# Performance work log

Measured on AMD Instinct MI355X. Metric: run time of the kernel, lower is better.

The kernel has to match this reference:

```python
import jax, jax.numpy as jnp
import numpy as np

HEADS = 8
NEG_SLOPE = 0.2


def _leaky(x):
    return jnp.where(x >= 0, x, NEG_SLOPE * x)


def _layernorm(x, g, b):
    # torch nn.LayerNorm over last dim, eps=1e-5, biased variance
    m = x.mean(-1, keepdims=True)
    v = ((x - m) ** 2).mean(-1, keepdims=True)
    return (x - m) / jnp.sqrt(v + 1e-5) * g + b


def _batchnorm(x, g, b):
    # training-mode BatchNorm2d, eps=1e-4, biased variance over (N,H,W)
    m = x.mean((0, 2, 3), keepdims=True)
    v = ((x - m) ** 2).mean((0, 2, 3), keepdims=True)
    return (x - m) / jnp.sqrt(v + 1e-4) * g[None, :, None, None] + b[None, :, None, None]


def _depthwise3x3(x, k):
    # x: (B,C,H,W), k: (C,1,3,3) depthwise kernel
    C = x.shape[1]
    return jax.lax.conv_general_dilated(
        x, k, (1, 1), 'SAME', feature_group_count=C,
        dimension_numbers=('NCHW', 'OIHW', 'NCHW'))


def _attn_layer(x, wq, wk, wv, wproj, bproj, wpos):
    # x: (B,H,W,C) channels-last; MDTA-style transposed attention
    b, H, W, C = x.shape
    d = C // HEADS
    xf = x.reshape(b, H * W, C)
    q, k, v = xf @ wq, xf @ wk, xf @ wv  # (b, n, C)

    def split(t):
        return t.reshape(b, H * W, HEADS, d).transpose(0, 2, 3, 1)  # (b, h, d, n)

    qh, kh, vh = split(q), split(k), split(v)
    # F.normalize over token axis n (eps=1e-12)
    qn = qh / jnp.maximum(jnp.sqrt((qh * qh).sum(-1, keepdims=True)), 1e-12)
    kn = kh / jnp.maximum(jnp.sqrt((kh * kh).sum(-1, keepdims=True)), 1e-12)
    attn = jax.nn.softmax(jnp.einsum('bhdn,bhen->bhde', kn, qn), axis=-1)  # (b,h,d,d)
    o = jnp.einsum('bhde,bhen->bhdn', attn, vh)  # (b,h,d,n)
    o = o.transpose(0, 3, 1, 2).reshape(b, H * W, C)
    out_c = (o @ wproj + bproj).reshape(b, H, W, C)
    out_p = _depthwise3x3(v.reshape(b, H, W, C).transpose(0, 3, 1, 2), wpos).transpose(0, 2, 3, 1)
    return out_c * out_p


def _transformer_block(x, wq, wk, wv, wproj, bproj, wpos, ln_g, ln_b, wff):
    # x: NCHW -> BHWC, 2 (attn + prenorm-FF) residual blocks, -> NCHW
    x = x.transpose(0, 2, 3, 1)
    for i in range(wq.shape[0]):
        x = _attn_layer(x, wq[i], wk[i], wv[i], wproj[i], bproj[i], wpos[i]) + x
        x = _layernorm(x, ln_g[i], ln_b[i]) @ wff[i] + x
    return x.transpose(0, 3, 1, 2)


def _saa(x, w1, w2):
    # SAA_Block: 8x8 spatial pool, global min-max norm, bmm correlation, SE gating
    b, c, H, W = x.shape
    y = x.reshape(b, c, 8, H // 8, 8, W // 8).mean((3, 5)).reshape(b, c, 64)
    y = (y - y.min()) / (y.max() - y.min())
    y = jnp.einsum('bci,bdi->bcd', y, y).mean(2)[:, :, None, None]  # (b,c,1,1)
    g = (x * y).mean((2, 3))  # (b,c) global avg pool
    g = jax.nn.sigmoid(_leaky(g @ w1) @ w2)
    return x * g[:, :, None, None]


def setup_inputs() -> dict:
    key = jax.random.key(0)
    B, C, H, W = 16, 64, 128, 128
    L = 2  # num_blocks in Transformer_block
    ks = jax.random.split(key, 12)
    s = 0.05
    inp = {
        'x': jax.random.normal(ks[0], (B, C, H, W), jnp.float32),
        'wq': jax.random.normal(ks[1], (L, C, C), jnp.float32) * s,
        'wk': jax.random.normal(ks[2], (L, C, C), jnp.float32) * s,
        'wv': jax.random.normal(ks[3], (L, C, C), jnp.float32) * s,
        'wproj': jax.random.normal(ks[4], (L, C, C), jnp.float32) * s,
        'bproj': jnp.zeros((L, C), jnp.float32),
        'wpos': jax.random.normal(ks[5], (L, C, 1, 3, 3), jnp.float32) * s,
        'ln_g': jnp.ones((L, C), jnp.float32),
        'ln_b': jnp.zeros((L, C), jnp.float32),
        'wff': jax.random.normal(ks[6], (L, C, C), jnp.float32) * s,
        'bn1_g': jnp.ones((C,), jnp.float32),
        'bn1_b': jnp.zeros((C,), jnp.float32),
        'wd': jax.random.normal(ks[7], (C, C), jnp.float32) * s,
        'bn2_g': jnp.ones((C,), jnp.float32),
        'bn2_b': jnp.zeros((C,), jnp.float32),
        'saa_w1': jax.random.normal(ks[8], (C, C // 16), jnp.float32) * s,
        'saa_w2': jax.random.normal(ks[9], (C // 16, C), jnp.float32) * s,
    }
    return inp


def reference(x, wq, wk, wv, wproj, bproj, wpos, ln_g, ln_b, wff,
              bn1_g, bn1_b, wd, bn2_g, bn2_b, saa_w1, saa_w2):
    # res path: C (Transformer_block) -> L -> B -> D (1x1 conv) -> L -> B
    r = _transformer_block(x, wq, wk, wv, wproj, bproj, wpos, ln_g, ln_b, wff)
    r = _batchnorm(_leaky(r), bn1_g, bn1_b)
    r = jnp.einsum('bchw,co->bohw', r, wd)  # 1x1 conv, bias=False
    r = _batchnorm(_leaky(r), bn2_g, bn2_b)
    return _saa(r + x, saa_w1, saa_w2)
```

## Files before the change

kernel.cpp:

```cpp
#include <hip/hip_runtime.h>

constexpr int NB = 16, NC = 64, NH = 128, NW = 128;
constexpr int NPIX = NH * NW;
constexpr int NTOT = NB * NPIX;
constexpr size_t BUF = (size_t)NTOT * NC;

constexpr size_t OFF_A   = 0;
constexpr size_t OFF_ACT = BUF;
constexpr size_t OFF_V   = 2 * BUF;
constexpr size_t OFF_S   = 3 * BUF;
constexpr size_t OFF_QSQ = OFF_S   + 2*16*512;
constexpr size_t OFF_KSQ = OFF_QSQ + 2048;
constexpr size_t OFF_BN1 = OFF_KSQ + 2048;
constexpr size_t OFF_BN2 = OFF_BN1 + 128;
constexpr size_t ZERO_FLOATS = 16384 + 2048 + 2048 + 128 + 128;
constexpr size_t OFF_W2  = OFF_BN2 + 128;
constexpr size_t OFF_AB1 = OFF_W2  + 131072;
constexpr size_t OFF_AB2 = OFF_AB1 + 128;
constexpr size_t OFF_Y   = OFF_AB2 + 128;
constexpr size_t OFF_GATE= OFF_Y   + 65536;

__device__ __forceinline__ float leaky(float x) { return x >= 0.f ? x : 0.2f * x; }

__global__ __launch_bounds__(256) void k_transpose_in(const float* __restrict__ x,
                                                      float* __restrict__ A) {
  __shared__ float t[64][65];
  int blk = blockIdx.x;
  int b = blk >> 8;
  int p0 = (blk & 255) * 64;
  int tid = threadIdx.x;
  int cq = tid >> 6, p = tid & 63;
  for (int i = 0; i < 16; i++) {
    int c = cq * 16 + i;
    t[p][c] = x[((size_t)(b * 64 + c)) * NPIX + p0 + p];
  }
  __syncthreads();
  int pq = tid >> 6, c = tid & 63;
  for (int i = 0; i < 16; i++) {
    int p2 = pq * 16 + i;
    A[((size_t)(b * NPIX + p0 + p2)) * 64 + c] = t[p2][c];
  }
}

__global__ __launch_bounds__(256) void k_mat_v(const float* __restrict__ act,
                                               const float* __restrict__ wv,
                                               float* __restrict__ v, int l) {
  int gpix = blockIdx.x * 256 + threadIdx.x;
  const float* xr = act + (size_t)gpix * 64;
  const float* W = wv + (size_t)l * 4096;
  float* out = v + (size_t)gpix * 64;
#pragma unroll 1
  for (int jc = 0; jc < 4; jc++) {
    float acc[16];
#pragma unroll
    for (int j = 0; j < 16; j++) acc[j] = 0.f;
#pragma unroll 1
    for (int cc = 0; cc < 4; cc++) {
      const float4 x0 = *(const float4*)(xr + cc * 16);
      const float4 x1 = *(const float4*)(xr + cc * 16 + 4);
      const float4 x2 = *(const float4*)(xr + cc * 16 + 8);
      const float4 x3 = *(const float4*)(xr + cc * 16 + 12);
      const float xv[16] = {x0.x,x0.y,x0.z,x0.w, x1.x,x1.y,x1.z,x1.w,
                            x2.x,x2.y,x2.z,x2.w, x3.x,x3.y,x3.z,x3.w};
#pragma unroll
      for (int ci = 0; ci < 16; ci++) {
        const float* wrow = W + (cc * 16 + ci) * 64 + jc * 16;
#pragma unroll
        for (int j = 0; j < 16; j++) acc[j] = fmaf(xv[ci], wrow[j], acc[j]);
      }
    }
    float4 o0 = {acc[0], acc[1], acc[2], acc[3]};
    float4 o1 = {acc[4], acc[5], acc[6], acc[7]};
    float4 o2 = {acc[8], acc[9], acc[10], acc[11]};
    float4 o3 = {acc[12], acc[13], acc[14], acc[15]};
    *(float4*)(out + jc * 16)      = o0;
    *(float4*)(out + jc * 16 + 4)  = o1;
    *(float4*)(out + jc * 16 + 8)  = o2;
    *(float4*)(out + jc * 16 + 12) = o3;
  }
}

__global__ __launch_bounds__(256) void k_qk_stats(const float* __restrict__ act,
    const float* __restrict__ wq, const float* __restrict__ wk,
    float* __restrict__ S, float* __restrict__ qsq, float* __restrict__ ksq, int l) {
  int wave = (blockIdx.x * 256 + threadIdx.x) >> 6;
  int lane = threadIdx.x & 63;
  int b = wave >> 7, hh = wave & 127;
  const float* Wq = wq + (size_t)l * 4096;
  const float* Wk = wk + (size_t)l * 4096;
  float wqc[64], wkc[64];
#pragma unroll
  for (int ci = 0; ci < 64; ci++) {
    wqc[ci] = Wq[ci * 64 + lane];
    wkc[ci] = Wk[ci * 64 + lane];
  }
  float Sacc[8];
#pragma unroll
  for (int e = 0; e < 8; e++) Sacc[e] = 0.f;
  float qsa = 0.f, ksa = 0.f;
  int gbase = lane & 56;
  const float* rowp = act + ((size_t)(b * NPIX + hh * NW)) * 64;
#pragma unroll 1
  for (int w = 0; w < 128; w++) {
    const float* xp = rowp + w * 64;
    float q = 0.f, k = 0.f;
#pragma unroll
    for (int ci = 0; ci < 64; ci++) {
      float xv = xp[ci];
      q = fmaf(xv, wqc[ci], q);
      k = fmaf(xv, wkc[ci], k);
    }
    qsa = fmaf(q, q, qsa);
    ksa = fmaf(k, k, ksa);
#pragma unroll
    for (int e = 0; e < 8; e++) {
      float qe = __shfl(q, gbase + e, 64);
      Sacc[e] = fmaf(k, qe, Sacc[e]);
    }
  }
  float* Sb = S + ((size_t)l * 16 + b) * 512 + lane * 8;
#pragma unroll
  for (int e = 0; e < 8; e++) atomicAdd(Sb + e, Sacc[e]);
  atomicAdd(qsq + ((size_t)l * 16 + b) * 64 + lane, qsa);
  atomicAdd(ksq + ((size_t)l * 16 + b) * 64 + lane, ksa);
}

__global__ __launch_bounds__(64) void k_attn(const float* __restrict__ S,
    const float* __restrict__ qsq, const float* __restrict__ ksq,
    const float* __restrict__ wproj, float* __restrict__ W2, int l) {
  int b = blockIdx.x, t = threadIdx.x;
  __shared__ float A[8][8][8];
  const float* Sb = S + ((size_t)l * 16 + b) * 512;
  const float* qs = qsq + ((size_t)l * 16 + b) * 64;
  const float* ks = ksq + ((size_t)l * 16 + b) * 64;
  int h = t >> 3, d = t & 7;
  float kden = fmaxf(sqrtf(ks[h * 8 + d]), 1e-12f);
  float pre[8];
  float mx = -1e30f;
#pragma unroll
  for (int e = 0; e < 8; e++) {
    float qden = fmaxf(sqrtf(qs[h * 8 + e]), 1e-12f);
    pre[e] = Sb[(h * 8 + d) * 8 + e] / (kden * qden);
    mx = fmaxf(mx, pre[e]);
  }
  float sum = 0.f;
#pragma unroll
  for (int e = 0; e < 8; e++) { pre[e] = expf(pre[e] - mx); sum += pre[e]; }
  float inv = 1.f / sum;
#pragma unroll
  for (int e = 0; e < 8; e++) A[h][d][e] = pre[e] * inv;
  __syncthreads();
  int co = t;
  const float* wp = wproj + (size_t)l * 4096;
  float* W2b = W2 + ((size_t)l * 16 + b) * 4096;
#pragma unroll 1
  for (int cin = 0; cin < 64; cin++) {
    int hh2 = cin >> 3, e = cin & 7;
    float acc = 0.f;
#pragma unroll
    for (int dd = 0; dd < 8; dd++)
      acc = fmaf(A[hh2][dd][e], wp[(hh2 * 8 + dd) * 64 + co], acc);
    W2b[cin * 64 + co] = acc;
  }
}

__global__ __launch_bounds__(128) void k_attnout_ff(
    const float* __restrict__ v, const float* __restrict__ actin,
    float* __restrict__ actout, const float* __restrict__ W2all,
    const float* __restrict__ bproj, const float* __restrict__ wpos,
    const float* __restrict__ lng, const float* __restrict__ lnb,
    const float* __restrict__ wff, int l) {
  __shared__ float ylds[128][65];
  __shared__ float wpl[9][64];
  int tid = threadIdx.x;
  for (int i = tid; i < 576; i += 128) {
    int c = i / 9, kk = i % 9;
    wpl[kk][c] = wpos[(size_t)l * 576 + i];
  }
  __syncthreads();
  int gpix = blockIdx.x * 128 + tid;
  int b = gpix >> 14;
  int p = gpix & 16383;
  int hh = p >> 7, ww = p & 127;
  const float* W2 = W2all + ((size_t)l * 16 + b) * 4096;
  const float* vr = v + (size_t)gpix * 64;
  const float* ar = actin + (size_t)gpix * 64;
  const float* bp = bproj + l * 64;
  float s1 = 0.f, s2 = 0.f;
#pragma unroll 1
  for (int jc = 0; jc < 4; jc++) {
    float acc[16];
#pragma unroll
    for (int j = 0; j < 16; j++) acc[j] = bp[jc * 16 + j];
#pragma unroll 1
    for (int cc = 0; cc < 4; cc++) {
      const float4 x0 = *(const float4*)(vr + cc * 16);
      const float4 x1 = *(const float4*)(vr + cc * 16 + 4);
      const float4 x2 = *(const float4*)(vr + cc * 16 + 8);
      const float4 x3 = *(const float4*)(vr + cc * 16 + 12);
      const float xv[16] = {x0.x,x0.y,x0.z,x0.w, x1.x,x1.y,x1.z,x1.w,
                            x2.x,x2.y,x2.z,x2.w, x3.x,x3.y,x3.z,x3.w};
#pragma unroll
      for (int ci = 0; ci < 16; ci++) {
        const float* wrow = W2 + (cc * 16 + ci) * 64 + jc * 16;
#pragma unroll
        for (int j = 0; j < 16; j++) acc[j] = fmaf(xv[ci], wrow[j], acc[j]);
      }
    }
    float op[16];
#pragma unroll
    for (int j = 0; j < 16; j++) op[j] = 0.f;
#pragma unroll 1
    for (int dy = -1; dy <= 1; dy++) {
#pragma unroll 1
      for (int dx = -1; dx <= 1; dx++) {
        bool ok = ((unsigned)(hh + dy) < 128u) && ((unsigned)(ww + dx) < 128u);
        const float* np = vr + (dy * NW + dx) * 64 + jc * 16;
        float4 n0 = {0,0,0,0}, n1 = {0,0,0,0}, n2 = {0,0,0,0}, n3 = {0,0,0,0};
        if (ok) {
          n0 = *(const float4*)(np);
          n1 = *(const float4*)(np + 4);
          n2 = *(const float4*)(np + 8);
          n3 = *(const float4*)(np + 12);
        }
        const float nv[16] = {n0.x,n0.y,n0.z,n0.w, n1.x,n1.y,n1.z,n1.w,
                              n2.x,n2.y,n2.z,n2.w, n3.x,n3.y,n3.z,n3.w};
        int kk = (dy + 1) * 3 + (dx + 1);
#pragma unroll
        for (int j = 0; j < 16; j++)
          op[j] = fmaf(nv[j], wpl[kk][jc * 16 + j], op[j]);
      }
    }
    const float4 a0 = *(const float4*)(ar + jc * 16);
    const float4 a1 = *(const float4*)(ar + jc * 16 + 4);
    const float4 a2 = *(const float4*)(ar + jc * 16 + 8);
    const float4 a3 = *(const float4*)(ar + jc * 16 + 12);
    const float av[16] = {a0.x,a0.y,a0.z,a0.w, a1.x,a1.y,a1.z,a1.w,
                          a2.x,a2.y,a2.z,a2.w, a3.x,a3.y,a3.z,a3.w};
#pragma unroll
    for (int j = 0; j < 16; j++) {
      float yv = acc[j] * op[j] + av[j];
      ylds[tid][jc * 16 + j] = yv;
      s1 += yv;
      s2 = fmaf(yv, yv, s2);
    }
  }
  float m = s1 * (1.f / 64.f);
  float var = s2 * (1.f / 64.f) - m * m;
  float iv = 1.f / sqrtf(var + 1e-5f);
  const float* G = lng + l * 64;
  const float* Bb = lnb + l * 64;
  const float* WF = wff + (size_t)l * 4096;
  float* aout = actout + (size_t)gpix * 64;
#pragma unroll 1
  for (int jc = 0; jc < 4; jc++) {
    float acc[16];
#pragma unroll
    for (int j = 0; j < 16; j++) acc[j] = ylds[tid][jc * 16 + j];
#pragma unroll 1
    for (int cc = 0; cc < 4; cc++) {
#pragma unroll
      for (int ci = 0; ci < 16; ci++) {
        int cin = cc * 16 + ci;
        float yn = (ylds[tid][cin] - m) * iv * G[cin] + Bb[cin];
        const float* wrow = WF + cin * 64 + jc * 16;
#pragma unroll
        for (int j = 0; j < 16; j++) acc[j] = fmaf(yn, wrow[j], acc[j]);
      }
    }
    float4 o0 = {acc[0], acc[1], acc[2], acc[3]};
    float4 o1 = {acc[4], acc[5], acc[6], acc[7]};
    float4 o2 = {acc[8], acc[9], acc[10], acc[11]};
    float4 o3 = {acc[12], acc[13], acc[14], acc[15]};
    *(float4*)(aout + jc * 16)      = o0;
    *(float4*)(aout + jc * 16 + 4)  = o1;
    *(float4*)(aout + jc * 16 + 8)  = o2;
    *(float4*)(aout + jc * 16 + 12) = o3;
  }
}

__global__ __launch_bounds__(256) void k_chanreduce(const float* __restrict__ in,
                                                    float* __restrict__ sums,
                                                    int mode) {
  int tid = threadIdx.x;
  int c = tid & 63;
  float s = 0.f, s2 = 0.f;
  size_t stride = (size_t)gridDim.x * blockDim.x;
  for (size_t idx = (size_t)blockIdx.x * blockDim.x + tid; idx < BUF; idx += stride) {
    float vv = in[idx];
    if (mode == 0) vv = leaky(vv);
    s += vv;
    s2 = fmaf(vv, vv, s2);
  }
  __shared__ float r1[256], r2[256];
  r1[tid] = s; r2[tid] = s2;
  __syncthreads();
  if (tid < 64) {
    s  = r1[tid] + r1[tid + 64] + r1[tid + 128] + r1[tid + 192];
    s2 = r2[tid] + r2[tid + 64] + r2[tid + 128] + r2[tid + 192];
    atomicAdd(&sums[c], s);
    atomicAdd(&sums[64 + c], s2);
  }
}

__global__ __launch_bounds__(64) void k_bnfin(const float* __restrict__ sums,
                                              const float* __restrict__ g,
                                              const float* __restrict__ bt,
                                              float* __restrict__ ab, float eps) {
  int c = threadIdx.x;
  float m = sums[c] * (1.f / (float)NTOT);
  float v = sums[64 + c] * (1.f / (float)NTOT) - m * m;
  float a = g[c] / sqrtf(v + eps);
  ab[c] = a;
  ab[64 + c] = bt[c] - m * a;
}

__global__ __launch_bounds__(256) void k_conv1x1(const float* __restrict__ act,
    const float* __restrict__ ab, const float* __restrict__ wd,
    float* __restrict__ out) {
  int gpix = blockIdx.x * 256 + threadIdx.x;
  const float* xr = act + (size_t)gpix * 64;
  float* o = out + (size_t)gpix * 64;
#pragma unroll 1
  for (int jc = 0; jc < 4; jc++) {
    float acc[16];
#pragma unroll
    for (int j = 0; j < 16; j++) acc[j] = 0.f;
#pragma unroll 1
    for (int cc = 0; cc < 4; cc++) {
      const float4 x0 = *(const float4*)(xr + cc * 16);
      const float4 x1 = *(const float4*)(xr + cc * 16 + 4);
      const float4 x2 = *(const float4*)(xr + cc * 16 + 8);
      const float4 x3 = *(const float4*)(xr + cc * 16 + 12);
      const float xv[16] = {x0.x,x0.y,x0.z,x0.w, x1.x,x1.y,x1.z,x1.w,
                            x2.x,x2.y,x2.z,x2.w, x3.x,x3.y,x3.z,x3.w};
#pragma unroll
      for (int ci = 0; ci < 16; ci++) {
        int cin = cc * 16 + ci;
        float t = fmaf(ab[cin], leaky(xv[ci]), ab[64 + cin]);
        const float* wrow = wd + cin * 64 + jc * 16;
#pragma unroll
        for (int j = 0; j < 16; j++) acc[j] = fmaf(t, wrow[j], acc[j]);
      }
    }
    float4 o0 = {leaky(acc[0]), leaky(acc[1]), leaky(acc[2]), leaky(acc[3])};
    float4 o1 = {leaky(acc[4]), leaky(acc[5]), leaky(acc[6]), leaky(acc[7])};
    float4 o2 = {leaky(acc[8]), leaky(acc[9]), leaky(acc[10]), leaky(acc[11])};
    float4 o3 = {leaky(acc[12]), leaky(acc[13]), leaky(acc[14]), leaky(acc[15])};
    *(float4*)(o + jc * 16)      = o0;
    *(float4*)(o + jc * 16 + 4)  = o1;
    *(float4*)(o + jc * 16 + 8)  = o2;
    *(float4*)(o + jc * 16 + 12) = o3;
  }
}

__global__ __launch_bounds__(512) void k_pool(const float* __restrict__ lr2,
    const float* __restrict__ xA, const float* __restrict__ ab2,
    float* __restrict__ y) {
  int blk = blockIdx.x;
  int b = blk >> 4;
  int br = (blk >> 1) & 7;
  int half = blk & 1;
  int t = threadIdx.x;
  int c = t & 63;
  int w8 = t >> 6;
  float a2 = ab2[c], b2 = ab2[64 + c];
  float acc[4];
#pragma unroll
  for (int i = 0; i < 4; i++) acc[i] = 0.f;
#pragma unroll 1
  for (int r = 0; r < 16; r++) {
    size_t base = ((size_t)(b * NPIX + (br * 16 + r) * NW + half * 64)) * 64;
#pragma unroll
    for (int i = 0; i < 8; i++) {
      size_t idx = base + (size_t)i * 512 + t;
      float sv = fmaf(a2, lr2[idx], b2) + xA[idx];
      acc[i >> 1] += sv;
    }
  }
  __shared__ float red[8][4][64];
#pragma unroll
  for (int i = 0; i < 4; i++) red[w8][i][c] = acc[i];
  __syncthreads();
  if (t < 256) {
    int bin = t >> 6, c2 = t & 63;
    float s = 0.f;
#pragma unroll
    for (int w = 0; w < 8; w++) s += red[w][bin][c2];
    y[((size_t)(b * 64 + c2)) * 64 + br * 8 + half * 4 + bin] = s * (1.f / 256.f);
  }
}

__global__ __launch_bounds__(1024) void k_saa(const float* __restrict__ y,
    const float* __restrict__ w1, const float* __restrict__ w2,
    float* __restrict__ gate) {
  int t = threadIdx.x;
  __shared__ float rmin[1024], rmax[1024];
  float mn = 1e30f, mx = -1e30f;
#pragma unroll 1
  for (int i = 0; i < 64; i++) {
    float vv = y[(size_t)i * 1024 + t];
    mn = fminf(mn, vv);
    mx = fmaxf(mx, vv);
  }
  rmin[t] = mn; rmax[t] = mx;
  __syncthreads();
  for (int s = 512; s > 0; s >>= 1) {
    if (t < s) {
      rmin[t] = fminf(rmin[t], rmin[t + s]);
      rmax[t] = fmaxf(rmax[t], rmax[t + s]);
    }
    __syncthreads();
  }
  float gmn = rmin[0], gmx = rmax[0];
  float inv = 1.f / (gmx - gmn);
  __syncthreads();
  int b = t >> 6;
  int i6 = t & 63;
  __shared__ float tl[16][64];
  {
    const float* yb = y + (size_t)b * 4096;
    float s = 0.f;
#pragma unroll 1
    for (int cl = 0; cl < 64; cl++) s += yb[cl * 64 + i6];
    tl[b][i6] = (s - 64.f * gmn) * inv;
  }
  __syncthreads();
  int cc = i6;
  const float* yc = y + (size_t)b * 4096 + cc * 64;
  float z = 0.f, ms = 0.f;
#pragma unroll 1
  for (int ii = 0; ii < 64; ii++) {
    float yr = yc[ii];
    z = fmaf((yr - gmn) * inv, tl[b][ii], z);
    ms += yr;
  }
  z *= (1.f / 64.f);
  ms *= (1.f / 64.f);
  __shared__ float g0l[16][64];
  g0l[b][cc] = z * ms;
  __syncthreads();
  __shared__ float hl[16][4];
  if (t < 64) {
    int bb = t >> 2, j = t & 3;
    float h = 0.f;
#pragma unroll 1
    for (int c2 = 0; c2 < 64; c2++) h = fmaf(g0l[bb][c2], w1[c2 * 4 + j], h);
    hl[bb][j] = leaky(h);
  }
  __syncthreads();
  float acc = 0.f;
#pragma unroll
  for (int j = 0; j < 4; j++) acc = fmaf(hl[b][j], w2[j * 64 + cc], acc);
  gate[t] = 1.f / (1.f + expf(-acc));
}

__global__ __launch_bounds__(256) void k_out(const float* __restrict__ lr2,
    const float* __restrict__ xA, const float* __restrict__ ab2,
    const float* __restrict__ gate, float* __restrict__ out) {
  __shared__ float tile[64][65];
  int blk = blockIdx.x;
  int b = blk >> 8;
  int p0 = (blk & 255) * 64;
  int tid = threadIdx.x;
  int c = tid & 63, pq = tid >> 6;
  float a2 = ab2[c], b2 = ab2[64 + c];
  for (int i = 0; i < 16; i++) {
    int p = pq * 16 + i;
    size_t idx = ((size_t)(b * NPIX + p0 + p)) * 64 + c;
    tile[p][c] = fmaf(a2, lr2[idx], b2) + xA[idx];
  }
  __syncthreads();
  int p = tid & 63, cq = tid >> 6;
  for (int i = 0; i < 16; i++) {
    int c2 = cq * 16 + i;
    out[((size_t)(b * 64 + c2)) * NPIX + p0 + p] = tile[p][c2] * gate[b * 64 + c2];
  }
}

extern "C" void kernel_launch(void* const* d_in, const int* in_sizes, int n_in,
                              void* d_out, int out_size, void* d_ws, size_t ws_size,
                              hipStream_t stream) {
  const float* x     = (const float*)d_in[0];
  const float* wq    = (const float*)d_in[1];
  const float* wk    = (const float*)d_in[2];
  const float* wv    = (const float*)d_in[3];
  const float* wproj = (const float*)d_in[4];
  const float* bproj = (const float*)d_in[5];
  const float* wpos  = (const float*)d_in[6];
  const float* ln_g  = (const float*)d_in[7];
  const float* ln_b  = (const float*)d_in[8];
  const float* wff   = (const float*)d_in[9];
  const float* bn1_g = (const float*)d_in[10];
  const float* bn1_b = (const float*)d_in[11];
  const float* wd    = (const float*)d_in[12];
  const float* bn2_g = (const float*)d_in[13];
  const float* bn2_b = (const float*)d_in[14];
  const float* sw1   = (const float*)d_in[15];
  const float* sw2   = (const float*)d_in[16];

  float* ws   = (float*)d_ws;
  float* A    = ws + OFF_A;
  float* ACT  = ws + OFF_ACT;
  float* V    = ws + OFF_V;
  float* S    = ws + OFF_S;
  float* QSQ  = ws + OFF_QSQ;
  float* KSQ  = ws + OFF_KSQ;
  float* BN1S = ws + OFF_BN1;
  float* BN2S = ws + OFF_BN2;
  float* W2   = ws + OFF_W2;
  float* AB1  = ws + OFF_AB1;
  float* AB2  = ws + OFF_AB2;
  float* Y    = ws + OFF_Y;
  float* GATE = ws + OFF_GATE;

  hipMemsetAsync((void*)S, 0, ZERO_FLOATS * sizeof(float), stream);

  k_transpose_in<<<4096, 256, 0, stream>>>(x, A);

  for (int l = 0; l < 2; l++) {
    const float* in = (l == 0) ? A : ACT;
    k_mat_v<<<NTOT / 256, 256, 0, stream>>>(in, wv, V, l);
    k_qk_stats<<<512, 256, 0, stream>>>(in, wq, wk, S, QSQ, KSQ, l);
    k_attn<<<16, 64, 0, stream>>>(S, QSQ, KSQ, wproj, W2, l);
    k_attnout_ff<<<NTOT / 128, 128, 0, stream>>>(V, in, ACT, W2, bproj, wpos,
                                                 ln_g, ln_b, wff, l);
  }

  k_chanreduce<<<512, 256, 0, stream>>>(ACT, BN1S, 0);
  k_bnfin<<<1, 64, 0, stream>>>(BN1S, bn1_g, bn1_b, AB1, 1e-4f);
  k_conv1x1<<<NTOT / 256, 256, 0, stream>>>(ACT, AB1, wd, V);
  k_chanreduce<<<512, 256, 0, stream>>>(V, BN2S, 1);
  k_bnfin<<<1, 64, 0, stream>>>(BN2S, bn2_g, bn2_b, AB2, 1e-4f);
  k_pool<<<256, 512, 0, stream>>>(V, A, AB2, Y);
  k_saa<<<1, 1024, 0, stream>>>(Y, sw1, sw2, GATE);
  k_out<<<4096, 256, 0, stream>>>(V, A, AB2, GATE, (float*)d_out);
}
```

Baseline: 1.514 ms.

## Fuse V with QK stats, restructure per-wave channel GEMMs, fold BN stats into producers

The separate V projection is merged into the QK-statistics kernel, so the activations are read once to produce q, k and v. The attention-output/FF and 1x1-conv kernels are rewritten wave-per-pixel-row: each lane holds one output channel's weight column in registers and broadcasts the input vector through a small LDS buffer. The depthwise conv uses a sliding 3x3 register window, and the BatchNorm channel sums are accumulated inside the producing kernels, which removes both chanreduce passes. This trades high register pressure (192 weight registers in k_qkv) and per-pixel cross-lane shuffles for LayerNorm against fewer full-tensor memory passes.

```diff
diff --git a/kernel.cpp b/kernel.cpp
--- a/kernel.cpp
+++ b/kernel.cpp
@@ -21,6 +21,7 @@
 constexpr size_t OFF_GATE= OFF_Y   + 65536;
 
 __device__ __forceinline__ float leaky(float x) { return x >= 0.f ? x : 0.2f * x; }
+#define RFL __builtin_amdgcn_readfirstlane
 
 __global__ __launch_bounds__(256) void k_transpose_in(const float* __restrict__ x,
                                                       float* __restrict__ A) {
@@ -42,73 +43,56 @@
   }
 }
 
-__global__ __launch_bounds__(256) void k_mat_v(const float* __restrict__ act,
-                                               const float* __restrict__ wv,
-                                               float* __restrict__ v, int l) {
-  int gpix = blockIdx.x * 256 + threadIdx.x;
-  const float* xr = act + (size_t)gpix * 64;
-  const float* W = wv + (size_t)l * 4096;
-  float* out = v + (size_t)gpix * 64;
-#pragma unroll 1
-  for (int jc = 0; jc < 4; jc++) {
-    float acc[16];
-#pragma unroll
-    for (int j = 0; j < 16; j++) acc[j] = 0.f;
-#pragma unroll 1
-    for (int cc = 0; cc < 4; cc++) {
-      const float4 x0 = *(const float4*)(xr + cc * 16);
-      const float4 x1 = *(const float4*)(xr + cc * 16 + 4);
-      const float4 x2 = *(const float4*)(xr + cc * 16 + 8);
-      const float4 x3 = *(const float4*)(xr + cc * 16 + 12);
-      const float xv[16] = {x0.x,x0.y,x0.z,x0.w, x1.x,x1.y,x1.z,x1.w,
-                            x2.x,x2.y,x2.z,x2.w, x3.x,x3.y,x3.z,x3.w};
-#pragma unroll
-      for (int ci = 0; ci < 16; ci++) {
-        const float* wrow = W + (cc * 16 + ci) * 64 + jc * 16;
-#pragma unroll
-        for (int j = 0; j < 16; j++) acc[j] = fmaf(xv[ci], wrow[j], acc[j]);
-      }
-    }
-    float4 o0 = {acc[0], acc[1], acc[2], acc[3]};
-    float4 o1 = {acc[4], acc[5], acc[6], acc[7]};
-    float4 o2 = {acc[8], acc[9], acc[10], acc[11]};
-    float4 o3 = {acc[12], acc[13], acc[14], acc[15]};
-    *(float4*)(out + jc * 16)      = o0;
-    *(float4*)(out + jc * 16 + 4)  = o1;
-    *(float4*)(out + jc * 16 + 8)  = o2;
-    *(float4*)(out + jc * 16 + 12) = o3;
-  }
-}
-
-__global__ __launch_bounds__(256) void k_qk_stats(const float* __restrict__ act,
+__global__ __launch_bounds__(256, 2) void k_qkv(const float* __restrict__ act,
     const float* __restrict__ wq, const float* __restrict__ wk,
-    float* __restrict__ S, float* __restrict__ qsq, float* __restrict__ ksq, int l) {
-  int wave = (blockIdx.x * 256 + threadIdx.x) >> 6;
-  int lane = threadIdx.x & 63;
-  int b = wave >> 7, hh = wave & 127;
+    const float* __restrict__ wv, float* __restrict__ v,
+    float* __restrict__ S, float* __restrict__ qsq, float* __restrict__ ksq,
+    int l) {
+  __shared__ float xb[8][64];
+  int tid = threadIdx.x;
+  int lane = tid & 63;
+  int wid = RFL((int)(blockIdx.x * 4 + (tid >> 6)));
+  int wslot = wid & 3;
+  int b = wid >> 8;
   const float* Wq = wq + (size_t)l * 4096;
   const float* Wk = wk + (size_t)l * 4096;
-  float wqc[64], wkc[64];
+  const float* Wv = wv + (size_t)l * 4096;
+  float wqc[64], wkc[64], wvc[64];
 #pragma unroll
   for (int ci = 0; ci < 64; ci++) {
     wqc[ci] = Wq[ci * 64 + lane];
     wkc[ci] = Wk[ci * 64 + lane];
+    wvc[ci] = Wv[ci * 64 + lane];
   }
   float Sacc[8];
 #pragma unroll
   for (int e = 0; e < 8; e++) Sacc[e] = 0.f;
   float qsa = 0.f, ksa = 0.f;
   int gbase = lane & 56;
-  const float* rowp = act + ((size_t)(b * NPIX + hh * NW)) * 64;
-#pragma unroll 1
-  for (int w = 0; w < 128; w++) {
-    const float* xp = rowp + w * 64;
-    float q = 0.f, k = 0.f;
-#pragma unroll
-    for (int ci = 0; ci < 64; ci++) {
-      float xv = xp[ci];
-      q = fmaf(xv, wqc[ci], q);
-      k = fmaf(xv, wkc[ci], k);
+  int base = wid * 4096;
+#pragma unroll 1
+  for (int p = 0; p < 64; p++) {
+    int off = base + p * 64;
+    float xl = act[off + lane];
+    int xs = wslot * 2 + (p & 1);
+    xb[xs][lane] = xl;
+    const float4* x4p = (const float4*)xb[xs];
+    float q = 0.f, k = 0.f, vv = 0.f;
+#pragma unroll
+    for (int i = 0; i < 16; i++) {
+      float4 x4 = x4p[i];
+      q  = fmaf(x4.x, wqc[4*i+0], q);
+      k  = fmaf(x4.x, wkc[4*i+0], k);
+      vv = fmaf(x4.x, wvc[4*i+0], vv);
+      q  = fmaf(x4.y, wqc[4*i+1], q);
+      k  = fmaf(x4.y, wkc[4*i+1], k);
+      vv = fmaf(x4.y, wvc[4*i+1], vv);
+      q  = fmaf(x4.z, wqc[4*i+2], q);
+      k  = fmaf(x4.z, wkc[4*i+2], k);
+      vv = fmaf(x4.z, wvc[4*i+2], vv);
+      q  = fmaf(x4.w, wqc[4*i+3], q);
+      k  = fmaf(x4.w, wkc[4*i+3], k);
+      vv = fmaf(x4.w, wvc[4*i+3], vv);
     }
     qsa = fmaf(q, q, qsa);
     ksa = fmaf(k, k, ksa);
@@ -117,6 +101,7 @@
       float qe = __shfl(q, gbase + e, 64);
       Sacc[e] = fmaf(k, qe, Sacc[e]);
     }
+    v[off + lane] = vv;
   }
   float* Sb = S + ((size_t)l * 16 + b) * 512 + lane * 8;
 #pragma unroll
@@ -164,142 +149,112 @@
   }
 }
 
-__global__ __launch_bounds__(128) void k_attnout_ff(
-    const float* __restrict__ v, const float* __restrict__ actin,
+__global__ __launch_bounds__(256, 2) void k_attnout_ff(
+    const float* __restrict__ vbuf, const float* __restrict__ actin,
     float* __restrict__ actout, const float* __restrict__ W2all,
     const float* __restrict__ bproj, const float* __restrict__ wpos,
     const float* __restrict__ lng, const float* __restrict__ lnb,
-    const float* __restrict__ wff, int l) {
-  __shared__ float ylds[128][65];
-  __shared__ float wpl[9][64];
+    const float* __restrict__ wff, float* __restrict__ bn1, int l, int dobn) {
+  __shared__ float xb[8][64], yb[8][64];
   int tid = threadIdx.x;
-  for (int i = tid; i < 576; i += 128) {
-    int c = i / 9, kk = i % 9;
-    wpl[kk][c] = wpos[(size_t)l * 576 + i];
-  }
-  __syncthreads();
-  int gpix = blockIdx.x * 128 + tid;
-  int b = gpix >> 14;
-  int p = gpix & 16383;
-  int hh = p >> 7, ww = p & 127;
+  int lane = tid & 63;
+  int bid = blockIdx.x;
+  int sbid = (bid & 7) * 128 + (bid >> 3);
+  int wid = RFL((int)(sbid * 4 + (tid >> 6)));
+  int wslot = wid & 3;
+  int b = wid >> 8;
+  int widb = wid & 255;
+  int hh = widb >> 1;
+  int c0 = (widb & 1) * 64;
   const float* W2 = W2all + ((size_t)l * 16 + b) * 4096;
-  const float* vr = v + (size_t)gpix * 64;
-  const float* ar = actin + (size_t)gpix * 64;
-  const float* bp = bproj + l * 64;
-  float s1 = 0.f, s2 = 0.f;
-#pragma unroll 1
-  for (int jc = 0; jc < 4; jc++) {
-    float acc[16];
-#pragma unroll
-    for (int j = 0; j < 16; j++) acc[j] = bp[jc * 16 + j];
-#pragma unroll 1
-    for (int cc = 0; cc < 4; cc++) {
-      const float4 x0 = *(const float4*)(vr + cc * 16);
-      const float4 x1 = *(const float4*)(vr + cc * 16 + 4);
-      const float4 x2 = *(const float4*)(vr + cc * 16 + 8);
-      const float4 x3 = *(const float4*)(vr + cc * 16 + 12);
-      const float xv[16] = {x0.x,x0.y,x0.z,x0.w, x1.x,x1.y,x1.z,x1.w,
-                            x2.x,x2.y,x2.z,x2.w, x3.x,x3.y,x3.z,x3.w};
-#pragma unroll
-      for (int ci = 0; ci < 16; ci++) {
-        const float* wrow = W2 + (cc * 16 + ci) * 64 + jc * 16;
-#pragma unroll
-        for (int j = 0; j < 16; j++) acc[j] = fmaf(xv[ci], wrow[j], acc[j]);
-      }
-    }
-    float op[16];
-#pragma unroll
-    for (int j = 0; j < 16; j++) op[j] = 0.f;
-#pragma unroll 1
-    for (int dy = -1; dy <= 1; dy++) {
-#pragma unroll 1
-      for (int dx = -1; dx <= 1; dx++) {
-        bool ok = ((unsigned)(hh + dy) < 128u) && ((unsigned)(ww + dx) < 128u);
-        const float* np = vr + (dy * NW + dx) * 64 + jc * 16;
-        float4 n0 = {0,0,0,0}, n1 = {0,0,0,0}, n2 = {0,0,0,0}, n3 = {0,0,0,0};
-        if (ok) {
-          n0 = *(const float4*)(np);
-          n1 = *(const float4*)(np + 4);
-          n2 = *(const float4*)(np + 8);
-          n3 = *(const float4*)(np + 12);
-        }
-        const float nv[16] = {n0.x,n0.y,n0.z,n0.w, n1.x,n1.y,n1.z,n1.w,
-                              n2.x,n2.y,n2.z,n2.w, n3.x,n3.y,n3.z,n3.w};
-        int kk = (dy + 1) * 3 + (dx + 1);
-#pragma unroll
-        for (int j = 0; j < 16; j++)
-          op[j] = fmaf(nv[j], wpl[kk][jc * 16 + j], op[j]);
-      }
-    }
-    const float4 a0 = *(const float4*)(ar + jc * 16);
-    const float4 a1 = *(const float4*)(ar + jc * 16 + 4);
-    const float4 a2 = *(const float4*)(ar + jc * 16 + 8);
-    const float4 a3 = *(const float4*)(ar + jc * 16 + 12);
-    const float av[16] = {a0.x,a0.y,a0.z,a0.w, a1.x,a1.y,a1.z,a1.w,
-                          a2.x,a2.y,a2.z,a2.w, a3.x,a3.y,a3.z,a3.w};
-#pragma unroll
-    for (int j = 0; j < 16; j++) {
-      float yv = acc[j] * op[j] + av[j];
-      ylds[tid][jc * 16 + j] = yv;
-      s1 += yv;
-      s2 = fmaf(yv, yv, s2);
-    }
-  }
-  float m = s1 * (1.f / 64.f);
-  float var = s2 * (1.f / 64.f) - m * m;
-  float iv = 1.f / sqrtf(var + 1e-5f);
-  const float* G = lng + l * 64;
-  const float* Bb = lnb + l * 64;
   const float* WF = wff + (size_t)l * 4096;
-  float* aout = actout + (size_t)gpix * 64;
-#pragma unroll 1
-  for (int jc = 0; jc < 4; jc++) {
-    float acc[16];
-#pragma unroll
-    for (int j = 0; j < 16; j++) acc[j] = ylds[tid][jc * 16 + j];
-#pragma unroll 1
-    for (int cc = 0; cc < 4; cc++) {
-#pragma unroll
-      for (int ci = 0; ci < 16; ci++) {
-        int cin = cc * 16 + ci;
-        float yn = (ylds[tid][cin] - m) * iv * G[cin] + Bb[cin];
-        const float* wrow = WF + cin * 64 + jc * 16;
-#pragma unroll
-        for (int j = 0; j < 16; j++) acc[j] = fmaf(yn, wrow[j], acc[j]);
-      }
-    }
-    float4 o0 = {acc[0], acc[1], acc[2], acc[3]};
-    float4 o1 = {acc[4], acc[5], acc[6], acc[7]};
-    float4 o2 = {acc[8], acc[9], acc[10], acc[11]};
-    float4 o3 = {acc[12], acc[13], acc[14], acc[15]};
-    *(float4*)(aout + jc * 16)      = o0;
-    *(float4*)(aout + jc * 16 + 4)  = o1;
-    *(float4*)(aout + jc * 16 + 8)  = o2;
-    *(float4*)(aout + jc * 16 + 12) = o3;
-  }
-}
-
-__global__ __launch_bounds__(256) void k_chanreduce(const float* __restrict__ in,
-                                                    float* __restrict__ sums,
-                                                    int mode) {
-  int tid = threadIdx.x;
-  int c = tid & 63;
-  float s = 0.f, s2 = 0.f;
-  size_t stride = (size_t)gridDim.x * blockDim.x;
-  for (size_t idx = (size_t)blockIdx.x * blockDim.x + tid; idx < BUF; idx += stride) {
-    float vv = in[idx];
-    if (mode == 0) vv = leaky(vv);
-    s += vv;
-    s2 = fmaf(vv, vv, s2);
-  }
-  __shared__ float r1[256], r2[256];
-  r1[tid] = s; r2[tid] = s2;
-  __syncthreads();
-  if (tid < 64) {
-    s  = r1[tid] + r1[tid + 64] + r1[tid + 128] + r1[tid + 192];
-    s2 = r2[tid] + r2[tid + 64] + r2[tid + 128] + r2[tid + 192];
-    atomicAdd(&sums[c], s);
-    atomicAdd(&sums[64 + c], s2);
+  float w2c[64], wfc[64];
+#pragma unroll
+  for (int ci = 0; ci < 64; ci++) {
+    w2c[ci] = W2[ci * 64 + lane];
+    wfc[ci] = WF[ci * 64 + lane];
+  }
+  float wpc[9];
+#pragma unroll
+  for (int kk = 0; kk < 9; kk++) wpc[kk] = wpos[(size_t)l * 576 + lane * 9 + kk];
+  float bp = bproj[l * 64 + lane];
+  float G  = lng[l * 64 + lane];
+  float Bb = lnb[l * 64 + lane];
+
+  bool okm = (hh > 0), okp = (hh < 127);
+  int base = wid * 4096;
+  float Lm = 0.f, L0 = 0.f, Lp = 0.f, Cm = 0.f, C0, Cp = 0.f;
+  C0 = vbuf[base + lane];
+  if (okm) Cm = vbuf[base - 8192 + lane];
+  if (okp) Cp = vbuf[base + 8192 + lane];
+  if (c0 == 64) {
+    L0 = vbuf[base - 64 + lane];
+    if (okm) Lm = vbuf[base - 64 - 8192 + lane];
+    if (okp) Lp = vbuf[base - 64 + 8192 + lane];
+  }
+  float s_bn = 0.f, s2_bn = 0.f;
+#pragma unroll 1
+  for (int p = 0; p < 64; p++) {
+    int off = base + p * 64;
+    float Rm = 0.f, R0 = 0.f, Rp = 0.f;
+    bool okc = (c0 + p + 1 < 128);
+    if (okc) {
+      R0 = vbuf[off + 64 + lane];
+      if (okm) Rm = vbuf[off + 64 - 8192 + lane];
+      if (okp) Rp = vbuf[off + 64 + 8192 + lane];
+    }
+    int xs = wslot * 2 + (p & 1);
+    xb[xs][lane] = C0;
+    const float4* x4p = (const float4*)xb[xs];
+    float a0 = 0.f, a1 = 0.f, a2 = 0.f, a3 = 0.f;
+#pragma unroll
+    for (int i = 0; i < 16; i++) {
+      float4 x4 = x4p[i];
+      a0 = fmaf(x4.x, w2c[4*i+0], a0);
+      a1 = fmaf(x4.y, w2c[4*i+1], a1);
+      a2 = fmaf(x4.z, w2c[4*i+2], a2);
+      a3 = fmaf(x4.w, w2c[4*i+3], a3);
+    }
+    float acc = (a0 + a1) + (a2 + a3) + bp;
+    float op = Lm * wpc[0] + Cm * wpc[1] + Rm * wpc[2]
+             + L0 * wpc[3] + C0 * wpc[4] + R0 * wpc[5]
+             + Lp * wpc[6] + Cp * wpc[7] + Rp * wpc[8];
+    float av = actin[off + lane];
+    float y = acc * op + av;
+    float t1 = y, t2 = y * y;
+#pragma unroll
+    for (int m = 1; m < 64; m <<= 1) {
+      t1 += __shfl_xor(t1, m, 64);
+      t2 += __shfl_xor(t2, m, 64);
+    }
+    float mean = t1 * (1.f / 64.f);
+    float var = t2 * (1.f / 64.f) - mean * mean;
+    float iv = 1.f / sqrtf(var + 1e-5f);
+    float yn = (y - mean) * iv * G + Bb;
+    yb[xs][lane] = yn;
+    const float4* y4p = (const float4*)yb[xs];
+    float o0 = 0.f, o1 = 0.f, o2 = 0.f, o3 = 0.f;
+#pragma unroll
+    for (int i = 0; i < 16; i++) {
+      float4 y4 = y4p[i];
+      o0 = fmaf(y4.x, wfc[4*i+0], o0);
+      o1 = fmaf(y4.y, wfc[4*i+1], o1);
+      o2 = fmaf(y4.z, wfc[4*i+2], o2);
+      o3 = fmaf(y4.w, wfc[4*i+3], o3);
+    }
+    float out = y + (o0 + o1) + (o2 + o3);
+    if (dobn) {
+      float lo = leaky(out);
+      s_bn += lo;
+      s2_bn = fmaf(lo, lo, s2_bn);
+    }
+    actout[off + lane] = out;
+    Lm = Cm; L0 = C0; Lp = Cp;
+    Cm = Rm; C0 = R0; Cp = Rp;
+  }
+  if (dobn) {
+    atomicAdd(&bn1[lane], s_bn);
+    atomicAdd(&bn1[64 + lane], s2_bn);
   }
 }
 
@@ -315,43 +270,44 @@
   ab[64 + c] = bt[c] - m * a;
 }
 
-__global__ __launch_bounds__(256) void k_conv1x1(const float* __restrict__ act,
+__global__ __launch_bounds__(256, 4) void k_conv1x1(const float* __restrict__ act,
     const float* __restrict__ ab, const float* __restrict__ wd,
-    float* __restrict__ out) {
-  int gpix = blockIdx.x * 256 + threadIdx.x;
-  const float* xr = act + (size_t)gpix * 64;
-  float* o = out + (size_t)gpix * 64;
-#pragma unroll 1
-  for (int jc = 0; jc < 4; jc++) {
-    float acc[16];
-#pragma unroll
-    for (int j = 0; j < 16; j++) acc[j] = 0.f;
-#pragma unroll 1
-    for (int cc = 0; cc < 4; cc++) {
-      const float4 x0 = *(const float4*)(xr + cc * 16);
-      const float4 x1 = *(const float4*)(xr + cc * 16 + 4);
-      const float4 x2 = *(const float4*)(xr + cc * 16 + 8);
-      const float4 x3 = *(const float4*)(xr + cc * 16 + 12);
-      const float xv[16] = {x0.x,x0.y,x0.z,x0.w, x1.x,x1.y,x1.z,x1.w,
-                            x2.x,x2.y,x2.z,x2.w, x3.x,x3.y,x3.z,x3.w};
-#pragma unroll
-      for (int ci = 0; ci < 16; ci++) {
-        int cin = cc * 16 + ci;
-        float t = fmaf(ab[cin], leaky(xv[ci]), ab[64 + cin]);
-        const float* wrow = wd + cin * 64 + jc * 16;
-#pragma unroll
-        for (int j = 0; j < 16; j++) acc[j] = fmaf(t, wrow[j], acc[j]);
-      }
-    }
-    float4 o0 = {leaky(acc[0]), leaky(acc[1]), leaky(acc[2]), leaky(acc[3])};
-    float4 o1 = {leaky(acc[4]), leaky(acc[5]), leaky(acc[6]), leaky(acc[7])};
-    float4 o2 = {leaky(acc[8]), leaky(acc[9]), leaky(acc[10]), leaky(acc[11])};
-    float4 o3 = {leaky(acc[12]), leaky(acc[13]), leaky(acc[14]), leaky(acc[15])};
-    *(float4*)(o + jc * 16)      = o0;
-    *(float4*)(o + jc * 16 + 4)  = o1;
-    *(float4*)(o + jc * 16 + 8)  = o2;
-    *(float4*)(o + jc * 16 + 12) = o3;
-  }
+    float* __restrict__ outv, float* __restrict__ bn2) {
+  __shared__ float xb[8][64];
+  int tid = threadIdx.x;
+  int lane = tid & 63;
+  int wid = RFL((int)(blockIdx.x * 4 + (tid >> 6)));
+  int wslot = wid & 3;
+  float wdc[64];
+#pragma unroll
+  for (int ci = 0; ci < 64; ci++) wdc[ci] = wd[ci * 64 + lane];
+  float a1l = ab[lane], b1l = ab[64 + lane];
+  float s_bn = 0.f, s2_bn = 0.f;
+  int base = wid * 4096;
+#pragma unroll 1
+  for (int p = 0; p < 64; p++) {
+    int off = base + p * 64;
+    float xl = act[off + lane];
+    float tl = fmaf(a1l, leaky(xl), b1l);
+    int xs = wslot * 2 + (p & 1);
+    xb[xs][lane] = tl;
+    const float4* x4p = (const float4*)xb[xs];
+    float a0 = 0.f, a1 = 0.f, a2 = 0.f, a3 = 0.f;
+#pragma unroll
+    for (int i = 0; i < 16; i++) {
+      float4 x4 = x4p[i];
+      a0 = fmaf(x4.x, wdc[4*i+0], a0);
+      a1 = fmaf(x4.y, wdc[4*i+1], a1);
+      a2 = fmaf(x4.z, wdc[4*i+2], a2);
+      a3 = fmaf(x4.w, wdc[4*i+3], a3);
+    }
+    float out = leaky((a0 + a1) + (a2 + a3));
+    s_bn += out;
+    s2_bn = fmaf(out, out, s2_bn);
+    outv[off + lane] = out;
+  }
+  atomicAdd(&bn2[lane], s_bn);
+  atomicAdd(&bn2[64 + lane], s2_bn);
 }
 
 __global__ __launch_bounds__(512) void k_pool(const float* __restrict__ lr2,
@@ -419,10 +375,10 @@
   int i6 = t & 63;
   __shared__ float tl[16][64];
   {
-    const float* yb = y + (size_t)b * 4096;
+    const float* yb2 = y + (size_t)b * 4096;
     float s = 0.f;
 #pragma unroll 1
-    for (int cl = 0; cl < 64; cl++) s += yb[cl * 64 + i6];
+    for (int cl = 0; cl < 64; cl++) s += yb2[cl * 64 + i6];
     tl[b][i6] = (s - 64.f * gmn) * inv;
   }
   __syncthreads();
@@ -520,17 +476,14 @@
 
   for (int l = 0; l < 2; l++) {
     const float* in = (l == 0) ? A : ACT;
-    k_mat_v<<<NTOT / 256, 256, 0, stream>>>(in, wv, V, l);
-    k_qk_stats<<<512, 256, 0, stream>>>(in, wq, wk, S, QSQ, KSQ, l);
+    k_qkv<<<1024, 256, 0, stream>>>(in, wq, wk, wv, V, S, QSQ, KSQ, l);
     k_attn<<<16, 64, 0, stream>>>(S, QSQ, KSQ, wproj, W2, l);
-    k_attnout_ff<<<NTOT / 128, 128, 0, stream>>>(V, in, ACT, W2, bproj, wpos,
-                                                 ln_g, ln_b, wff, l);
-  }
-
-  k_chanreduce<<<512, 256, 0, stream>>>(ACT, BN1S, 0);
+    k_attnout_ff<<<1024, 256, 0, stream>>>(V, in, ACT, W2, bproj, wpos,
+                                           ln_g, ln_b, wff, BN1S, l, l == 1);
+  }
+
   k_bnfin<<<1, 64, 0, stream>>>(BN1S, bn1_g, bn1_b, AB1, 1e-4f);
-  k_conv1x1<<<NTOT / 256, 256, 0, stream>>>(ACT, AB1, wd, V);
-  k_chanreduce<<<512, 256, 0, stream>>>(V, BN2S, 1);
+  k_conv1x1<<<1024, 256, 0, stream>>>(ACT, AB1, wd, V, BN2S);
   k_bnfin<<<1, 64, 0, stream>>>(BN2S, bn2_g, bn2_b, AB2, 1e-4f);
   k_pool<<<256, 512, 0, stream>>>(V, A, AB2, Y);
   k_saa<<<1, 1024, 0, stream>>>(Y, sw1, sw2, GATE);
```

After: 1.321 ms. 12.7% less time.
